# Kernel tuning notes

Measured on AMD Instinct MI355X. Metric: run time of the kernel, lower is better.

## Reference

```python
import jax, jax.numpy as jnp
import numpy as np

HEAD_DIM = 128
NEG = -1e9


def setup_inputs() -> dict:
    key = jax.random.key(0)
    kq, kk, kv, kl = jax.random.split(key, 4)
    B, S, D = 8, 2048, HEAD_DIM
    q = jax.random.normal(kq, (B, S, D), dtype=jnp.float32)
    k = jax.random.normal(kk, (B, S, D), dtype=jnp.float32)
    v = jax.random.normal(kv, (B, S, D), dtype=jnp.float32)
    event_length = jax.random.randint(kl, (B,), 0, 2048, dtype=jnp.int32)
    return {"q": q, "k": k, "v": v, "event_length": event_length}


def reference(q, k, v, event_length):
    B, S, D = q.shape
    scale = jnp.sqrt(jnp.asarray(D, dtype=q.dtype))
    # [B, S, S] attention scores
    scores = jnp.einsum("bsd,btd->bst", q, k) / scale
    idx = jnp.arange(S)
    valid = idx[None, :] < event_length[:, None]          # [B, S]
    mask = valid[:, :, None] & valid[:, None, :]          # [B, S, S]
    scores = jnp.where(mask, scores, jnp.asarray(NEG, dtype=scores.dtype))
    attn = jax.nn.softmax(scores, axis=-1)
    # dropout is eval-mode identity
    return jnp.einsum("bst,btd->bsd", attn, v)
```

## Files before the change

kernel.cpp:

```cpp
#include <hip/hip_runtime.h>

#define S 2048
#define D 128
#define BATCH 8
#define NS 4
#define KSTR 136
#define VSTR 72

typedef _Float16 half8 __attribute__((ext_vector_type(8)));
typedef _Float16 half4_t __attribute__((ext_vector_type(4)));
typedef float f4 __attribute__((ext_vector_type(4)));

__device__ __forceinline__ half8 cvt8(f4 a, f4 b) {
    half8 h;
    h[0] = (_Float16)a[0]; h[1] = (_Float16)a[1];
    h[2] = (_Float16)a[2]; h[3] = (_Float16)a[3];
    h[4] = (_Float16)b[0]; h[5] = (_Float16)b[1];
    h[6] = (_Float16)b[2]; h[7] = (_Float16)b[3];
    return h;
}

__global__ __launch_bounds__(256) void k_prep(const float* __restrict__ kin,
                                              const float* __restrict__ v,
                                              _Float16* __restrict__ kh,
                                              _Float16* __restrict__ vt,
                                              float* __restrict__ vpart) {
    int bid = blockIdx.x;
    int b = bid & 7, c = bid >> 3, tid = threadIdx.x;
    size_t off = ((size_t)b * S + c * 16) * D;
    {
        size_t i = (size_t)tid * 8;
        f4 a = *(const f4*)(kin + off + i);
        f4 bb = *(const f4*)(kin + off + i + 4);
        *(half8*)(kh + off + i) = cvt8(a, bb);
    }
    __shared__ float tile[16 * 132];
    __shared__ f4 sred[256][2];
    int d0 = (tid & 15) * 8, t = tid >> 4;
    f4 x = *(const f4*)(v + off + (size_t)t * D + d0);
    f4 y = *(const f4*)(v + off + (size_t)t * D + d0 + 4);
    *(f4*)&tile[t * 132 + d0] = x;
    *(f4*)&tile[t * 132 + d0 + 4] = y;
    sred[tid][0] = x; sred[tid][1] = y;
    __syncthreads();
    if (tid < 16) {
        f4 s0 = sred[tid][0], s1 = sred[tid][1];
        for (int g = 1; g < 16; ++g) { s0 += sred[g * 16 + tid][0]; s1 += sred[g * 16 + tid][1]; }
        float* dst = vpart + ((size_t)b * 128 + c) * 128 + tid * 8;
        *(f4*)dst = s0;
        *(f4*)(dst + 4) = s1;
    }
    int u = tid & 1, dd = tid >> 1;
    half8 h;
    #pragma unroll
    for (int i2 = 0; i2 < 8; ++i2) h[i2] = (_Float16)tile[(u * 8 + i2) * 132 + dd];
    *(half8*)(vt + ((size_t)(b * D + dd)) * S + c * 16 + u * 8) = h;
}

__global__ __launch_bounds__(256, 4) void k_attn(
    const float* __restrict__ q, const _Float16* __restrict__ kh,
    const _Float16* __restrict__ vt, const int* __restrict__ el,
    _Float16* __restrict__ part, float* __restrict__ stats) {
    int bid = blockIdx.x;
    int b = bid & 7, mg = (bid >> 3) & 31, j = bid >> 8;
    int Lb = el[b], m0 = mg * 64;
    if (m0 >= Lb) return;
    int nkt = (Lb + 63) >> 6;

    int tid = threadIdx.x, lane = tid & 63, w = tid >> 6;
    int col = lane & 15, quad = lane >> 4;

    __shared__ _Float16 Kh[64 * KSTR];
    __shared__ _Float16 Vt[128 * VSTR];

    const float scale = 0.0883883476483184f;
    half8 qf[4];
    {
        const float* qb = q + ((size_t)b * S + m0 + w * 16 + col) * D;
        #pragma unroll
        for (int kc = 0; kc < 4; ++kc) {
            f4 a = *(const f4*)(qb + kc * 32 + quad * 8);
            f4 b2 = *(const f4*)(qb + kc * 32 + quad * 8 + 4);
            a *= scale; b2 *= scale;
            qf[kc] = cvt8(a, b2);
        }
    }

    f4 O[8];
    #pragma unroll
    for (int i = 0; i < 8; ++i) O[i] = (f4){0.f, 0.f, 0.f, 0.f};
    float ps = 0.f;

    int kr = tid >> 4, kc8 = (tid & 15) << 3;
    int vr = tid >> 3, vc8 = (tid & 7) << 3;
    const _Float16* kb_ = kh + (size_t)b * S * D;
    const _Float16* vb_ = vt + (size_t)b * D * S;

    if (j < nkt) {
        half8 kreg[4], vreg[4];
        {
            int t0 = j * 64;
            #pragma unroll
            for (int p = 0; p < 4; ++p)
                kreg[p] = *(const half8*)(kb_ + (size_t)(t0 + p * 16 + kr) * D + kc8);
            #pragma unroll
            for (int p = 0; p < 4; ++p)
                vreg[p] = *(const half8*)(vb_ + (size_t)(p * 32 + vr) * S + t0 + vc8);
            #pragma unroll
            for (int p = 0; p < 4; ++p)
                *(half8*)&Kh[(p * 16 + kr) * KSTR + kc8] = kreg[p];
            #pragma unroll
            for (int p = 0; p < 4; ++p)
                *(half8*)&Vt[(p * 32 + vr) * VSTR + vc8] = vreg[p];
        }
        __syncthreads();

        for (int kt = j; kt < nkt; kt += NS) {
            int t0 = kt * 64;
            bool hasnext = (kt + NS) < nkt;
            if (hasnext) {
                int tn = t0 + NS * 64;
                #pragma unroll
                for (int p = 0; p < 4; ++p)
                    kreg[p] = *(const half8*)(kb_ + (size_t)(tn + p * 16 + kr) * D + kc8);
                #pragma unroll
                for (int p = 0; p < 4; ++p)
                    vreg[p] = *(const half8*)(vb_ + (size_t)(p * 32 + vr) * S + tn + vc8);
            }

            #pragma unroll
            for (int nt = 0; nt < 4; ++nt) {
                f4 sa = {0.f, 0.f, 0.f, 0.f};
                __builtin_amdgcn_s_setprio(1);
                #pragma unroll
                for (int kc = 0; kc < 4; ++kc) {
                    half8 kf = *(const half8*)&Kh[(nt * 16 + col) * KSTR + kc * 32 + quad * 8];
                    sa = __builtin_amdgcn_mfma_f32_16x16x32_f16(kf, qf[kc], sa, 0, 0, 0);
                }
                __builtin_amdgcn_s_setprio(0);
                int tq = t0 + nt * 16 + quad * 4;
                half4_t ph;
                #pragma unroll
                for (int r = 0; r < 4; ++r) {
                    float e = (tq + r < Lb) ? __expf(fminf(sa[r], 10.0f)) : 0.f;
                    ps += e;
                    ph[r] = (_Float16)e;
                }
                __builtin_amdgcn_s_setprio(1);
                #pragma unroll
                for (int dt = 0; dt < 8; ++dt) {
                    half4_t vf = *(const half4_t*)&Vt[(dt * 16 + col) * VSTR + nt * 16 + quad * 4];
                    O[dt] = __builtin_amdgcn_mfma_f32_16x16x16f16(ph, vf, O[dt], 0, 0, 0);
                }
                __builtin_amdgcn_s_setprio(0);
            }

            if (hasnext) {
                __syncthreads();
                #pragma unroll
                for (int p = 0; p < 4; ++p)
                    *(half8*)&Kh[(p * 16 + kr) * KSTR + kc8] = kreg[p];
                #pragma unroll
                for (int p = 0; p < 4; ++p)
                    *(half8*)&Vt[(p * 32 + vr) * VSTR + vc8] = vreg[p];
                __syncthreads();
            }
        }
    }

    ps += __shfl_xor(ps, 16, 64);
    ps += __shfl_xor(ps, 32, 64);
    size_t pbase = (size_t)(j * BATCH + b) * S;
    #pragma unroll
    for (int dt = 0; dt < 8; ++dt)
        #pragma unroll
        for (int r = 0; r < 4; ++r) {
            int row = m0 + w * 16 + quad * 4 + r;
            part[(pbase + row) * D + dt * 16 + col] = (_Float16)O[dt][r];
        }
    if (quad == 0) stats[pbase + m0 + w * 16 + col] = ps;
}

__global__ __launch_bounds__(256, 4) void k_comb(
    const _Float16* __restrict__ part, const float* __restrict__ stats,
    const float* __restrict__ vpart, const int* __restrict__ el,
    float* __restrict__ out) {
    int bid = blockIdx.x;
    int b = bid & 7, mg16 = bid >> 3;
    int L = el[b], m0 = mg16 * 16, tid = threadIdx.x;
    const float inv_s = 1.0f / (float)S;
    __shared__ float vsum[128];

    bool tail = (m0 + 16 > L);
    if (tail) {
        if (tid < 128) {
            float s = 0.f;
            const float* pp = vpart + (size_t)b * 128 * 128 + tid;
            #pragma unroll 4
            for (int c = 0; c < 128; ++c) s += pp[c * 128];
            vsum[tid] = s * inv_s;
        }
        __syncthreads();
    }

    int r = tid >> 4, d08 = (tid & 15) * 8;
    int srow = m0 + r;
    float* orow = out + ((size_t)b * S + srow) * D + d08;
    if (srow >= L) {
        *(f4*)orow = *(const f4*)(vsum + d08);
        *(f4*)(orow + 4) = *(const f4*)(vsum + d08 + 4);
        return;
    }
    size_t rbase = (size_t)b * S + srow;
    const size_t step = (size_t)BATCH * S;
    float l = 0.f;
    #pragma unroll
    for (int jj = 0; jj < NS; ++jj) l += stats[rbase + jj * step];
    float inv = 1.0f / l;
    f4 o0 = {0.f, 0.f, 0.f, 0.f}, o1 = {0.f, 0.f, 0.f, 0.f};
    #pragma unroll
    for (int jj = 0; jj < NS; ++jj) {
        half8 h = *(const half8*)(part + (rbase + jj * step) * D + d08);
        f4 x0 = {(float)h[0], (float)h[1], (float)h[2], (float)h[3]};
        f4 x1 = {(float)h[4], (float)h[5], (float)h[6], (float)h[7]};
        o0 += x0; o1 += x1;
    }
    *(f4*)orow = o0 * inv;
    *(f4*)(orow + 4) = o1 * inv;
}

extern "C" void kernel_launch(void* const* d_in, const int* in_sizes, int n_in,
                              void* d_out, int out_size, void* d_ws, size_t ws_size,
                              hipStream_t stream) {
    const float* q = (const float*)d_in[0];
    const float* k = (const float*)d_in[1];
    const float* v = (const float*)d_in[2];
    const int* el = (const int*)d_in[3];
    float* out = (float*)d_out;

    const size_t SZ_VPART = (size_t)BATCH * 128 * 128 * 4;
    const size_t SZ_HALF  = (size_t)BATCH * D * S * 2;
    const size_t SZ_STAT  = (size_t)NS * BATCH * S * 4;
    float* vpart = (float*)d_ws;
    _Float16* kh = (_Float16*)((char*)d_ws + SZ_VPART);
    _Float16* vt = (_Float16*)((char*)d_ws + SZ_VPART + SZ_HALF);
    float* stats = (float*)((char*)d_ws + SZ_VPART + 2 * SZ_HALF);
    _Float16* part = (_Float16*)((char*)d_ws + SZ_VPART + 2 * SZ_HALF + SZ_STAT);

    k_prep<<<dim3(1024), 256, 0, stream>>>(k, v, kh, vt, vpart);
    k_attn<<<dim3(1024), 256, 0, stream>>>(q, kh, vt, el, part, stats);
    k_comb<<<dim3(1024), 256, 0, stream>>>(part, stats, vpart, el, out);
}
```

Before: 114.6 us.

## Fuse K/V fp16 conversion and V transpose into attention kernel, drop prep pass

Removes the separate prep kernel that converted K to fp16 and transposed V into fp16 workspace buffers. The attention kernel now loads fp32 K and V directly, converts in registers, and transposes V while writing to shared memory. The V column sums needed for masked rows are computed by 32 extra blocks appended to the attention grid, which also shrinks the vpart reduction in the combine kernel. This saves one launch and a full write-and-read of the fp16 copies. In exchange each attention block re-reads fp32 K and V, which doubles the load bytes and repeats the conversion work across blocks, and V is now fetched with strided scalar loads.

```diff
diff --git a/kernel.cpp b/kernel.cpp
--- a/kernel.cpp
+++ b/kernel.cpp
@@ -6,6 +6,7 @@
 #define NS 4
 #define KSTR 136
 #define VSTR 72
+#define NATT 1024
 
 typedef _Float16 half8 __attribute__((ext_vector_type(8)));
 typedef _Float16 half4_t __attribute__((ext_vector_type(4)));
@@ -20,58 +21,50 @@
     return h;
 }
 
-__global__ __launch_bounds__(256) void k_prep(const float* __restrict__ kin,
-                                              const float* __restrict__ v,
-                                              _Float16* __restrict__ kh,
-                                              _Float16* __restrict__ vt,
-                                              float* __restrict__ vpart) {
-    int bid = blockIdx.x;
-    int b = bid & 7, c = bid >> 3, tid = threadIdx.x;
-    size_t off = ((size_t)b * S + c * 16) * D;
-    {
-        size_t i = (size_t)tid * 8;
-        f4 a = *(const f4*)(kin + off + i);
-        f4 bb = *(const f4*)(kin + off + i + 4);
-        *(half8*)(kh + off + i) = cvt8(a, bb);
-    }
-    __shared__ float tile[16 * 132];
-    __shared__ f4 sred[256][2];
-    int d0 = (tid & 15) * 8, t = tid >> 4;
-    f4 x = *(const f4*)(v + off + (size_t)t * D + d0);
-    f4 y = *(const f4*)(v + off + (size_t)t * D + d0 + 4);
-    *(f4*)&tile[t * 132 + d0] = x;
-    *(f4*)&tile[t * 132 + d0 + 4] = y;
-    sred[tid][0] = x; sred[tid][1] = y;
-    __syncthreads();
-    if (tid < 16) {
-        f4 s0 = sred[tid][0], s1 = sred[tid][1];
-        for (int g = 1; g < 16; ++g) { s0 += sred[g * 16 + tid][0]; s1 += sred[g * 16 + tid][1]; }
-        float* dst = vpart + ((size_t)b * 128 + c) * 128 + tid * 8;
-        *(f4*)dst = s0;
-        *(f4*)(dst + 4) = s1;
-    }
-    int u = tid & 1, dd = tid >> 1;
-    half8 h;
-    #pragma unroll
-    for (int i2 = 0; i2 < 8; ++i2) h[i2] = (_Float16)tile[(u * 8 + i2) * 132 + dd];
-    *(half8*)(vt + ((size_t)(b * D + dd)) * S + c * 16 + u * 8) = h;
-}
-
 __global__ __launch_bounds__(256, 4) void k_attn(
-    const float* __restrict__ q, const _Float16* __restrict__ kh,
-    const _Float16* __restrict__ vt, const int* __restrict__ el,
-    _Float16* __restrict__ part, float* __restrict__ stats) {
-    int bid = blockIdx.x;
+    const float* __restrict__ q, const float* __restrict__ kin,
+    const float* __restrict__ v, const int* __restrict__ el,
+    _Float16* __restrict__ part, float* __restrict__ stats,
+    float* __restrict__ vpart) {
+    int bid = blockIdx.x, tid = threadIdx.x;
+
+    __shared__ __align__(16) char smem[35840];
+
+    if (bid >= NATT) {
+        int cs = bid - NATT;
+        int b = cs & 7, seg = cs >> 3;
+        f4 a0 = {0.f, 0.f, 0.f, 0.f}, a1 = {0.f, 0.f, 0.f, 0.f};
+        int d0 = (tid & 15) * 8, tl = tid >> 4;
+        const float* vb = v + ((size_t)b * S + seg * 512) * D;
+        #pragma unroll 4
+        for (int it = 0; it < 32; ++it) {
+            const float* row = vb + (size_t)(it * 16 + tl) * D + d0;
+            a0 += *(const f4*)row;
+            a1 += *(const f4*)(row + 4);
+        }
+        f4 (*sred)[2] = (f4 (*)[2])smem;
+        sred[tid][0] = a0; sred[tid][1] = a1;
+        __syncthreads();
+        if (tid < 16) {
+            f4 s0 = sred[tid][0], s1 = sred[tid][1];
+            for (int g = 1; g < 16; ++g) { s0 += sred[g * 16 + tid][0]; s1 += sred[g * 16 + tid][1]; }
+            float* dst = vpart + ((size_t)b * 4 + seg) * 128 + tid * 8;
+            *(f4*)dst = s0;
+            *(f4*)(dst + 4) = s1;
+        }
+        return;
+    }
+
     int b = bid & 7, mg = (bid >> 3) & 31, j = bid >> 8;
     int Lb = el[b], m0 = mg * 64;
     if (m0 >= Lb) return;
     int nkt = (Lb + 63) >> 6;
 
-    int tid = threadIdx.x, lane = tid & 63, w = tid >> 6;
+    int lane = tid & 63, w = tid >> 6;
     int col = lane & 15, quad = lane >> 4;
 
-    __shared__ _Float16 Kh[64 * KSTR];
-    __shared__ _Float16 Vt[128 * VSTR];
+    _Float16* Kh = (_Float16*)smem;
+    _Float16* Vt = (_Float16*)(smem + 17408);
 
     const float scale = 0.0883883476483184f;
     half8 qf[4];
@@ -92,26 +85,36 @@
     float ps = 0.f;
 
     int kr = tid >> 4, kc8 = (tid & 15) << 3;
-    int vr = tid >> 3, vc8 = (tid & 7) << 3;
-    const _Float16* kb_ = kh + (size_t)b * S * D;
-    const _Float16* vb_ = vt + (size_t)b * D * S;
-
+    int dv = tid & 127, oct = tid >> 7;
+    const float* kb_ = kin + (size_t)b * S * D;
+    const float* vb_ = v + (size_t)b * S * D;
+
+    half8 kreg[4], vreg[4];
     if (j < nkt) {
-        half8 kreg[4], vreg[4];
         {
             int t0 = j * 64;
             #pragma unroll
-            for (int p = 0; p < 4; ++p)
-                kreg[p] = *(const half8*)(kb_ + (size_t)(t0 + p * 16 + kr) * D + kc8);
-            #pragma unroll
-            for (int p = 0; p < 4; ++p)
-                vreg[p] = *(const half8*)(vb_ + (size_t)(p * 32 + vr) * S + t0 + vc8);
+            for (int p = 0; p < 4; ++p) {
+                const float* kp = kb_ + (size_t)(t0 + p * 16 + kr) * D + kc8;
+                kreg[p] = cvt8(*(const f4*)kp, *(const f4*)(kp + 4));
+            }
+            #pragma unroll
+            for (int p = 0; p < 4; ++p) {
+                int o = p * 2 + oct;
+                const float* vp = vb_ + (size_t)(t0 + o * 8) * D + dv;
+                half8 h;
+                #pragma unroll
+                for (int i = 0; i < 8; ++i) h[i] = (_Float16)vp[(size_t)i * D];
+                vreg[p] = h;
+            }
             #pragma unroll
             for (int p = 0; p < 4; ++p)
                 *(half8*)&Kh[(p * 16 + kr) * KSTR + kc8] = kreg[p];
             #pragma unroll
-            for (int p = 0; p < 4; ++p)
-                *(half8*)&Vt[(p * 32 + vr) * VSTR + vc8] = vreg[p];
+            for (int p = 0; p < 4; ++p) {
+                int o = p * 2 + oct;
+                *(half8*)&Vt[dv * VSTR + o * 8] = vreg[p];
+            }
         }
         __syncthreads();
 
@@ -121,11 +124,19 @@
             if (hasnext) {
                 int tn = t0 + NS * 64;
                 #pragma unroll
-                for (int p = 0; p < 4; ++p)
-                    kreg[p] = *(const half8*)(kb_ + (size_t)(tn + p * 16 + kr) * D + kc8);
-                #pragma unroll
-                for (int p = 0; p < 4; ++p)
-                    vreg[p] = *(const half8*)(vb_ + (size_t)(p * 32 + vr) * S + tn + vc8);
+                for (int p = 0; p < 4; ++p) {
+                    const float* kp = kb_ + (size_t)(tn + p * 16 + kr) * D + kc8;
+                    kreg[p] = cvt8(*(const f4*)kp, *(const f4*)(kp + 4));
+                }
+                #pragma unroll
+                for (int p = 0; p < 4; ++p) {
+                    int o = p * 2 + oct;
+                    const float* vp = vb_ + (size_t)(tn + o * 8) * D + dv;
+                    half8 h;
+                    #pragma unroll
+                    for (int i = 0; i < 8; ++i) h[i] = (_Float16)vp[(size_t)i * D];
+                    vreg[p] = h;
+                }
             }
 
             #pragma unroll
@@ -161,8 +172,10 @@
                 for (int p = 0; p < 4; ++p)
                     *(half8*)&Kh[(p * 16 + kr) * KSTR + kc8] = kreg[p];
                 #pragma unroll
-                for (int p = 0; p < 4; ++p)
-                    *(half8*)&Vt[(p * 32 + vr) * VSTR + vc8] = vreg[p];
+                for (int p = 0; p < 4; ++p) {
+                    int o = p * 2 + oct;
+                    *(half8*)&Vt[dv * VSTR + o * 8] = vreg[p];
+                }
                 __syncthreads();
             }
         }
@@ -194,10 +207,8 @@
     bool tail = (m0 + 16 > L);
     if (tail) {
         if (tid < 128) {
-            float s = 0.f;
-            const float* pp = vpart + (size_t)b * 128 * 128 + tid;
-            #pragma unroll 4
-            for (int c = 0; c < 128; ++c) s += pp[c * 128];
+            const float* pp = vpart + (size_t)b * 4 * 128 + tid;
+            float s = pp[0] + pp[128] + pp[256] + pp[384];
             vsum[tid] = s * inv_s;
         }
         __syncthreads();
@@ -238,16 +249,12 @@
     const int* el = (const int*)d_in[3];
     float* out = (float*)d_out;
 
-    const size_t SZ_VPART = (size_t)BATCH * 128 * 128 * 4;
-    const size_t SZ_HALF  = (size_t)BATCH * D * S * 2;
+    const size_t SZ_VPART = (size_t)BATCH * 4 * 128 * 4;
     const size_t SZ_STAT  = (size_t)NS * BATCH * S * 4;
     float* vpart = (float*)d_ws;
-    _Float16* kh = (_Float16*)((char*)d_ws + SZ_VPART);
-    _Float16* vt = (_Float16*)((char*)d_ws + SZ_VPART + SZ_HALF);
-    float* stats = (float*)((char*)d_ws + SZ_VPART + 2 * SZ_HALF);
-    _Float16* part = (_Float16*)((char*)d_ws + SZ_VPART + 2 * SZ_HALF + SZ_STAT);
-
-    k_prep<<<dim3(1024), 256, 0, stream>>>(k, v, kh, vt, vpart);
-    k_attn<<<dim3(1024), 256, 0, stream>>>(q, kh, vt, el, part, stats);
+    float* stats = (float*)((char*)d_ws + SZ_VPART);
+    _Float16* part = (_Float16*)((char*)d_ws + SZ_VPART + SZ_STAT);
+
+    k_attn<<<dim3(NATT + 32), 256, 0, stream>>>(q, k, v, el, part, stats, vpart);
     k_comb<<<dim3(1024), 256, 0, stream>>>(part, stats, vpart, el, out);
 }
```

Result: faster. 106.9 us (-6.8%).
